# Kernel tuning notes

Hardware: AMD Instinct MI355X
Metric: run time of the kernel (lower is better)

Reference implementation:

```python
import jax, jax.numpy as jnp
import numpy as np

B, N, F_DIM, C_DIM, L = 4, 2048, 64, 64, 3

def setup_inputs() -> dict:
    key = jax.random.key(0)
    k1, k2, k3 = jax.random.split(key, 3)
    V = jax.random.normal(k1, (B, N, F_DIM), dtype=jnp.float32)
    A = jax.random.uniform(k2, (B, N, N, L), dtype=jnp.float32)
    h_weights = jax.random.normal(k3, (L + 1, C_DIM, F_DIM), dtype=jnp.float32) * 0.05
    return {"V": V, "A": A, "h_weights": h_weights}

def reference(V, A, h_weights):
    # Original math: A_aug = concat([I, A], -1)  (identity as edge-type 0)
    # H[b,i,j,c,f] = sum_l A_aug[b,i,j,l] * h_weights[l,c,f]
    # V_out[b,i,c] = sum_{j,f} H[b,i,j,c,f] * V[b,j,f]; relu.
    # The identity edge-type contributes h_weights[0] @ V[b,i] directly,
    # avoiding materializing the concatenated (B,N,N,L+1) tensor.
    self_term = jnp.einsum('cf,bif->bic', h_weights[0], V)        # (B,N,C)
    rel_term = jnp.einsum('bijl,lcf,bjf->bic', A, h_weights[1:], V)
    return jax.nn.relu(self_term + rel_term)
```

## Files before the change

### kernel.cpp

```cpp
#include <hip/hip_runtime.h>
#include <cstdint>

#define BDIM 4
#define NDIM 2048
#define FDIM 64
#define CDIM 64
#define LDIM 3
#define KTOT (NDIM * LDIM)
#define BK 256
#define NSTEP (KTOT / BK)
#define KB (KTOT / 32)
#define BSTEP (8 * 2048)
#define BTOT (KB * 2048)

typedef __attribute__((ext_vector_type(4))) float f32x4;
typedef __attribute__((ext_vector_type(8))) short s16x8;
typedef __attribute__((ext_vector_type(4))) unsigned int u32x4;

__device__ __forceinline__ unsigned short f2bf(float x) {
  union { float f; uint32_t u; } v; v.f = x;
  uint32_t r = v.u + 0x7FFFu + ((v.u >> 16) & 1u);
  return (unsigned short)(r >> 16);
}

__device__ __forceinline__ uint32_t cvtpk(float lo, float hi) {
  uint32_t r;
  asm("v_cvt_pk_bf16_f32 %0, %1, %2" : "=v"(r) : "v"(lo), "v"(hi));
  return r;
}

__global__ __launch_bounds__(64) void k1_precompute(
    const float* __restrict__ V, const float* __restrict__ hw,
    float* __restrict__ S, unsigned short* __restrict__ Ut3) {
  const int j0 = blockIdx.x * 16;
  const int le = blockIdx.y;
  const int b  = blockIdx.z;
  const int lane = threadIdx.x;
  const int q = lane & 15, g = lane >> 4;

  const float* vrow = V + ((size_t)(b * NDIM + j0 + q)) * FDIM + g * 8;
  f32x4 va0 = *(const f32x4*)(vrow);
  f32x4 va1 = *(const f32x4*)(vrow + 4);
  f32x4 va2 = *(const f32x4*)(vrow + 32);
  f32x4 va3 = *(const f32x4*)(vrow + 36);
  s16x8 a0, a1;
#pragma unroll
  for (int e = 0; e < 4; ++e) {
    a0[e]     = (short)f2bf(va0[e]);
    a0[e + 4] = (short)f2bf(va1[e]);
    a1[e]     = (short)f2bf(va2[e]);
    a1[e + 4] = (short)f2bf(va3[e]);
  }

  const float* hbase = hw + (size_t)le * CDIM * FDIM;
#pragma unroll
  for (int ct = 0; ct < 4; ++ct) {
    const float* hrow = hbase + (size_t)(ct * 16 + q) * FDIM + g * 8;
    f32x4 hb0 = *(const f32x4*)(hrow);
    f32x4 hb1 = *(const f32x4*)(hrow + 4);
    f32x4 hb2 = *(const f32x4*)(hrow + 32);
    f32x4 hb3 = *(const f32x4*)(hrow + 36);
    s16x8 b0, b1;
#pragma unroll
    for (int e = 0; e < 4; ++e) {
      b0[e]     = (short)f2bf(hb0[e]);
      b0[e + 4] = (short)f2bf(hb1[e]);
      b1[e]     = (short)f2bf(hb2[e]);
      b1[e + 4] = (short)f2bf(hb3[e]);
    }
    f32x4 acc = {0.f, 0.f, 0.f, 0.f};
    acc = __builtin_amdgcn_mfma_f32_16x16x32_bf16(a0, b0, acc, 0, 0, 0);
    acc = __builtin_amdgcn_mfma_f32_16x16x32_bf16(a1, b1, acc, 0, 0, 0);
    if (le == 0) {
#pragma unroll
      for (int rr = 0; rr < 4; ++rr) {
        int j = j0 + g * 4 + rr;
        S[((size_t)b * NDIM + j) * CDIM + ct * 16 + q] = acc[rr];
      }
    } else {
#pragma unroll
      for (int rr = 0; rr < 4; ++rr) {
        int j = j0 + g * 4 + rr;
        int k = j * 3 + (le - 1);
        int kb = k >> 5, gg = (k >> 3) & 3, ee = k & 7;
        size_t off = ((size_t)b * KB + kb) * 2048 + (size_t)ct * 512 +
                     (size_t)gg * 128 + (size_t)q * 8 + ee;
        Ut3[off] = f2bf(acc[rr]);
      }
    }
  }
}

__global__ __launch_bounds__(512) void k2_main(
    const float* __restrict__ A, const unsigned short* __restrict__ Ut3,
    const float* __restrict__ S, float* __restrict__ out) {
  __shared__ float Abuf[2][8192];

  const int bid = blockIdx.x;
  const int swz = (bid & 7) * 32 + (bid >> 3);
  const int b   = swz >> 6;
  const int i0  = (swz & 63) * 32;
  const int tid = threadIdx.x;
  const int lane = tid & 63, w = tid >> 6;
  const int q = lane & 15, g = lane >> 4, q7 = q & 7;
  const int wr = w >> 2, wc = w & 3;

  const float* agb[4];
#pragma unroll
  for (int t = 0; t < 4; ++t) {
    int r = 4 * w + t;
    agb[t] = A + ((size_t)(b * NDIM + i0 + r)) * KTOT + ((lane ^ (r & 7)) * 4);
  }
  int akoff = 0;

  const unsigned short* bgb =
      Ut3 + (size_t)b * BTOT + (size_t)wc * 512 + (size_t)lane * 8;
  int bkoff = 0;

  float* ldsw = &Abuf[0][0] + w * 1024 + lane * 4;

#define GLL4(slot)                                                            \
  do {                                                                        \
    __builtin_amdgcn_global_load_lds(                                         \
        (__attribute__((address_space(1))) void*)(agb[0] + akoff),            \
        (__attribute__((address_space(3))) void*)(ldsw + (slot) * 8192), 16, 0, 0); \
    __builtin_amdgcn_global_load_lds(                                         \
        (__attribute__((address_space(1))) void*)(agb[1] + akoff),            \
        (__attribute__((address_space(3))) void*)(ldsw + (slot) * 8192 + 256), 16, 0, 0); \
    __builtin_amdgcn_global_load_lds(                                         \
        (__attribute__((address_space(1))) void*)(agb[2] + akoff),            \
        (__attribute__((address_space(3))) void*)(ldsw + (slot) * 8192 + 512), 16, 0, 0); \
    __builtin_amdgcn_global_load_lds(                                         \
        (__attribute__((address_space(1))) void*)(agb[3] + akoff),            \
        (__attribute__((address_space(3))) void*)(ldsw + (slot) * 8192 + 768), 16, 0, 0); \
  } while (0)

#define LDB(BW, HB)                                                           \
  do {                                                                        \
    _Pragma("unroll")                                                         \
    for (int t = 0; t < 4; ++t)                                               \
      BW[t] = *(const s16x8*)(bgb + bkoff + (size_t)((HB) + t) * 2048);       \
  } while (0)

#define HALF(half, BR)                                                        \
  do {                                                                        \
    const float* rowp = &Abuf[s & 1][0] + (wr * 16 + q) * 256;                \
    _Pragma("unroll")                                                         \
    for (int kk = 0; kk < 4; ++kk) {                                          \
      int kg = (half) * 4 + kk;                                               \
      f32x4 a0 = *(const f32x4*)(rowp + ((kg * 8 + ((2 * g) ^ q7)) << 2));    \
      f32x4 a1 = *(const f32x4*)(rowp + ((kg * 8 + ((2 * g + 1) ^ q7)) << 2));\
      u32x4 wv;                                                               \
      wv[0] = cvtpk(a0[0], a0[1]); wv[1] = cvtpk(a0[2], a0[3]);               \
      wv[2] = cvtpk(a1[0], a1[1]); wv[3] = cvtpk(a1[2], a1[3]);               \
      if (kk & 1)                                                             \
        accB = __builtin_amdgcn_mfma_f32_16x16x32_bf16(                       \
            __builtin_bit_cast(s16x8, wv), BR[kk], accB, 0, 0, 0);            \
      else                                                                    \
        accA = __builtin_amdgcn_mfma_f32_16x16x32_bf16(                       \
            __builtin_bit_cast(s16x8, wv), BR[kk], accA, 0, 0, 0);            \
    }                                                                         \
  } while (0)

  f32x4 accA = {0.f, 0.f, 0.f, 0.f}, accB = {0.f, 0.f, 0.f, 0.f};
  s16x8 bA[4], bB[4];

  GLL4(0); akoff = BK;
  LDB(bA, 0);

  for (int s = 0; s < NSTEP; ++s) {
    LDB(bB, 4);
    GLL4((s + 1) & 1);
    if (s + 2 < NSTEP) akoff += BK;
    if (s + 1 < NSTEP) bkoff += BSTEP;
    asm volatile("s_waitcnt vmcnt(8)" ::: "memory");
    __builtin_amdgcn_sched_barrier(0);
    __builtin_amdgcn_s_barrier();
    __builtin_amdgcn_sched_barrier(0);
    HALF(0, bA);
    LDB(bA, 0);
    asm volatile("s_waitcnt vmcnt(8)" ::: "memory");
    __builtin_amdgcn_sched_barrier(0);
    HALF(1, bB);
    __builtin_amdgcn_s_barrier();
  }
#undef HALF
#undef GLL4
#undef LDB

  asm volatile("s_waitcnt vmcnt(0)" ::: "memory");

  f32x4 acc = accA + accB;
  const int c = wc * 16 + q;
#pragma unroll
  for (int rr = 0; rr < 4; ++rr) {
    int i = i0 + wr * 16 + g * 4 + rr;
    size_t idx = ((size_t)(b * NDIM) + i) * CDIM + c;
    float v = acc[rr] + S[idx];
    out[idx] = v > 0.f ? v : 0.f;
  }
}

extern "C" void kernel_launch(void* const* d_in, const int* in_sizes, int n_in,
                              void* d_out, int out_size, void* d_ws, size_t ws_size,
                              hipStream_t stream) {
  const float* V  = (const float*)d_in[0];
  const float* A  = (const float*)d_in[1];
  const float* hw = (const float*)d_in[2];
  float* out = (float*)d_out;

  float* S = (float*)d_ws;
  unsigned short* Ut3 =
      (unsigned short*)((char*)d_ws + (size_t)BDIM * NDIM * CDIM * sizeof(float));

  k1_precompute<<<dim3(NDIM / 16, LDIM + 1, BDIM), 64, 0, stream>>>(V, hw, S, Ut3);
  k2_main<<<dim3((NDIM / 32) * BDIM), 512, 0, stream>>>(A, Ut3, S, out);
}
```

Measured before the change: 46.52 us.

## Split K dimension in two across blocks and add a reduction kernel

The main GEMM now launches 512 blocks instead of 256, each handling half the reduction dimension and writing a partial result to a workspace buffer. A new third kernel sums the two partials with the self term and applies ReLU. The goal is to fill more of the GPU's compute units, since 256 blocks leaves the device underused. In exchange it adds an extra launch and extra global traffic for the partial buffers.

```diff
diff --git a/kernel.cpp b/kernel.cpp
--- a/kernel.cpp
+++ b/kernel.cpp
@@ -8,10 +8,12 @@
 #define LDIM 3
 #define KTOT (NDIM * LDIM)
 #define BK 256
-#define NSTEP (KTOT / BK)
+#define NSTEP 12
 #define KB (KTOT / 32)
 #define BSTEP (8 * 2048)
 #define BTOT (KB * 2048)
+#define BHALF (96 * 2048)
+#define TOTE (BDIM * NDIM * CDIM)
 
 typedef __attribute__((ext_vector_type(4))) float f32x4;
 typedef __attribute__((ext_vector_type(8))) short s16x8;
@@ -93,13 +95,15 @@
 
 __global__ __launch_bounds__(512) void k2_main(
     const float* __restrict__ A, const unsigned short* __restrict__ Ut3,
-    const float* __restrict__ S, float* __restrict__ out) {
+    float* __restrict__ P) {
   __shared__ float Abuf[2][8192];
 
   const int bid = blockIdx.x;
-  const int swz = (bid & 7) * 32 + (bid >> 3);
-  const int b   = swz >> 6;
-  const int i0  = (swz & 63) * 32;
+  const int swz = (bid & 7) * 64 + (bid >> 3);
+  const int h    = swz & 1;
+  const int rest = swz >> 1;
+  const int b    = rest >> 6;
+  const int i0   = (rest & 63) * 32;
   const int tid = threadIdx.x;
   const int lane = tid & 63, w = tid >> 6;
   const int q = lane & 15, g = lane >> 4, q7 = q & 7;
@@ -111,11 +115,11 @@
     int r = 4 * w + t;
     agb[t] = A + ((size_t)(b * NDIM + i0 + r)) * KTOT + ((lane ^ (r & 7)) * 4);
   }
-  int akoff = 0;
+  int akoff = h * (KTOT / 2);
 
   const unsigned short* bgb =
       Ut3 + (size_t)b * BTOT + (size_t)wc * 512 + (size_t)lane * 8;
-  int bkoff = 0;
+  int bkoff = h * BHALF;
 
   float* ldsw = &Abuf[0][0] + w * 1024 + lane * 4;
 
@@ -165,7 +169,7 @@
   f32x4 accA = {0.f, 0.f, 0.f, 0.f}, accB = {0.f, 0.f, 0.f, 0.f};
   s16x8 bA[4], bB[4];
 
-  GLL4(0); akoff = BK;
+  GLL4(0); akoff += BK;
   LDB(bA, 0);
 
   for (int s = 0; s < NSTEP; ++s) {
@@ -191,14 +195,27 @@
   asm volatile("s_waitcnt vmcnt(0)" ::: "memory");
 
   f32x4 acc = accA + accB;
+  float* Ph = P + (size_t)h * TOTE;
   const int c = wc * 16 + q;
 #pragma unroll
   for (int rr = 0; rr < 4; ++rr) {
     int i = i0 + wr * 16 + g * 4 + rr;
-    size_t idx = ((size_t)(b * NDIM) + i) * CDIM + c;
-    float v = acc[rr] + S[idx];
-    out[idx] = v > 0.f ? v : 0.f;
-  }
+    Ph[((size_t)(b * NDIM) + i) * CDIM + c] = acc[rr];
+  }
+}
+
+__global__ __launch_bounds__(256) void k3_reduce(
+    const float* __restrict__ S, const float* __restrict__ P,
+    float* __restrict__ out) {
+  const int idx = blockIdx.x * 1024 + threadIdx.x * 4;
+  f32x4 sv = *(const f32x4*)(S + idx);
+  f32x4 p0 = *(const f32x4*)(P + idx);
+  f32x4 p1 = *(const f32x4*)(P + TOTE + idx);
+  f32x4 v = sv + p0 + p1;
+  f32x4 o;
+#pragma unroll
+  for (int e = 0; e < 4; ++e) o[e] = v[e] > 0.f ? v[e] : 0.f;
+  *(f32x4*)(out + idx) = o;
 }
 
 extern "C" void kernel_launch(void* const* d_in, const int* in_sizes, int n_in,
@@ -211,8 +228,11 @@
 
   float* S = (float*)d_ws;
   unsigned short* Ut3 =
-      (unsigned short*)((char*)d_ws + (size_t)BDIM * NDIM * CDIM * sizeof(float));
+      (unsigned short*)((char*)d_ws + (size_t)TOTE * sizeof(float));
+  float* P = (float*)((char*)d_ws + (size_t)TOTE * sizeof(float) +
+                      (size_t)BDIM * BTOT * sizeof(unsigned short));
 
   k1_precompute<<<dim3(NDIM / 16, LDIM + 1, BDIM), 64, 0, stream>>>(V, hw, S, Ut3);
-  k2_main<<<dim3((NDIM / 32) * BDIM), 512, 0, stream>>>(A, Ut3, S, out);
-}
+  k2_main<<<dim3(512), 512, 0, stream>>>(A, Ut3, P);
+  k3_reduce<<<dim3(512), 256, 0, stream>>>(S, P, out);
+}
```

After: 48.86 us. 1.05x slower.
